# Performance work log

Measured on AMD Instinct MI355X. Metric: run time of the kernel, lower is better.

The kernel has to match this reference:

```python
import jax, jax.numpy as jnp
import numpy as np

MIN_LEN = 4      # g.min_word_length
MAX_LEN = 10     # g.max_word_length
THRESH = 0.05    # g.init_threshold
NEG = -1e9


def setup_inputs() -> dict:
    key = jax.random.key(0)
    ks = jax.random.split(key, 6)
    B, L, F, D, U, V = 16, 64, 60, 256, 600, 10000
    x = jax.random.normal(ks[0], (B, L, F), jnp.float32)            # batch dense feat matrix
    unit_feats = jax.random.normal(ks[1], (U, F), jnp.float32)      # per-unit features
    W = jax.random.normal(ks[2], (F, D), jnp.float32) * 0.1         # FeatEmbedding weight
    lengths = jax.random.randint(ks[3], (B,), MIN_LEN, L + 1)       # sentence lengths
    indexed_segments = jax.random.randint(ks[4], (V, MAX_LEN), 0, U)  # vocab -> unit ids
    vocab_length = jax.random.randint(ks[5], (V,), MIN_LEN, MAX_LEN + 1)
    return dict(x=x, unit_feats=unit_feats, W=W, lengths=lengths,
                indexed_segments=indexed_segments, vocab_length=vocab_length)


def reference(x, unit_feats, W, lengths, indexed_segments, vocab_length):
    B, L, _ = x.shape
    V, J = indexed_segments.shape
    # embedding: features -> char_emb space
    word_repr = x @ W                 # [B, L, D]
    unit_repr = unit_feats @ W        # [U, D]
    # cosine similarity between every segment position and every unit
    wn = word_repr / (jnp.linalg.norm(word_repr, axis=-1, keepdims=True) + 1e-8)
    un = unit_repr / (jnp.linalg.norm(unit_repr, axis=-1, keepdims=True) + 1e-8)
    sim = jnp.einsum('bld,ud->blu', wn, un)  # [B, L, U]
    # pad so span gathers past the end read zeros (masked later by `viable`)
    sim_pad = jnp.pad(sim, ((0, 0), (0, J), (0, 0)))
    # accumulate per-position unit scores along each vocab word's unit sequence
    acc = jnp.zeros((B, L, V), sim.dtype)
    per_len = []
    for j in range(J):  # fixed small loop over word-length positions
        # sim at start+j for unit indexed_segments[v, j] -> [B, L, V]
        s_j = sim_pad[:, j:j + L, :][:, :, indexed_segments[:, j]]
        acc = acc + s_j
        if j + 1 >= MIN_LEN:
            per_len.append(acc / (j + 1))  # length-normalized match score
    scores = jnp.stack(per_len, axis=2)  # [B, len_s=L, len_e=E, V]
    E = scores.shape[2]
    k = jnp.arange(E) + MIN_LEN                          # candidate word lengths
    ends = jnp.arange(L)[:, None] + k[None, :] - 1        # [L, E]
    viable = ends[None] < lengths[:, None, None]          # [B, L, E]
    len_match = vocab_length[None, None, None, :] == k[None, None, :, None]
    mask = viable[..., None] & len_match                  # [B, L, E, V]
    masked = jnp.where(mask, scores, NEG)
    # best vocab word per span candidate
    value = masked.max(axis=-1)                           # [B, L, E]
    matched_vocab = masked.argmax(axis=-1)                # [B, L, E]
    matched = value > THRESH
    # best span candidate per batch element (eval path: hard max)
    flat = value.reshape(B, -1)                           # [B, L*E]
    best_inds = flat.argmax(axis=-1)
    best_scores = flat.max(axis=-1)
    best_starts = best_inds // E
    best_ends = best_inds % E + best_starts + MIN_LEN - 1
    any_matched = matched.reshape(B, -1).any(axis=-1)
    best_vocab = jnp.take_along_axis(matched_vocab.reshape(B, -1), best_inds[:, None], axis=1)[:, 0]
    return best_scores, best_starts, best_ends, any_matched, best_vocab
```

## Files before the change

### kernel.cpp

```cpp
#include <hip/hip_runtime.h>
#include <math.h>

#define BB 16
#define LL 64
#define FF 60
#define DD 256
#define UU 600
#define VV 10000
#define JMAX 10
#define MINL 4
#define EE 7
#define NEG (-1e9f)
#define TH 0.05f
#define BCAP 10240

#define UNT_OFF   0
#define WNT_OFF   163840
#define SIM_OFF   425984
#define CNT_OFF   1040384
#define SRT_OFF   1040392
#define VAL_OFF   1613832
#define VOC_OFF   1628168

__global__ __launch_bounds__(256) void k_prep(const int* __restrict__ seg,
                                              const int* __restrict__ vlen,
                                              const float* __restrict__ x,
                                              const float* __restrict__ uf,
                                              const float* __restrict__ W,
                                              unsigned int* __restrict__ cnt,
                                              unsigned int* __restrict__ srt,
                                              float* __restrict__ unT,
                                              float* __restrict__ wnT) {
    __shared__ unsigned long long sP[4][2];
    __shared__ int wTab[4][8];
    __shared__ int sBase[8];
    int blk = blockIdx.x;
    if (blk < 40) {
        int tid  = threadIdx.x;
        int lane = tid & 63;
        int w    = tid >> 6;
        int v    = blk * 256 + tid;

        unsigned long long p0 = 0, p1 = 0;
        int lim = blk * 256;
        for (int i = tid; i < lim; i += 256) {
            int e2 = vlen[i] - MINL;
            if (e2 < 4) p0 += 1ull << (e2 * 16);
            else        p1 += 1ull << ((e2 - 4) * 16);
        }
#pragma unroll
        for (int m = 32; m > 0; m >>= 1) {
            p0 += __shfl_xor(p0, m, 64);
            p1 += __shfl_xor(p1, m, 64);
        }
        if (lane == 0) { sP[w][0] = p0; sP[w][1] = p1; }

        int e = (v < VV) ? (vlen[v] - MINL) : -1;
        unsigned long long below = (lane == 0) ? 0ull : (~0ull >> (64 - lane));
        unsigned long long mym = 0;
#pragma unroll
        for (int b2 = 0; b2 < EE; ++b2) {
            unsigned long long m = __ballot(e == b2);
            if (lane == 0) wTab[w][b2] = (int)__popcll(m);
            if (e == b2) mym = m;
        }
        __syncthreads();
        if (tid < EE) {
            unsigned long long q0 = sP[0][0] + sP[1][0] + sP[2][0] + sP[3][0];
            unsigned long long q1 = sP[0][1] + sP[1][1] + sP[2][1] + sP[3][1];
            int base = (tid < 4) ? (int)((q0 >> (tid * 16)) & 0xffffull)
                                 : (int)((q1 >> ((tid - 4) * 16)) & 0xffffull);
            sBase[tid] = base;
            if (blk == 39)
                cnt[tid] = (unsigned)(base + wTab[0][tid] + wTab[1][tid]
                                           + wTab[2][tid] + wTab[3][tid]);
        }
        __syncthreads();

        if (v < VV) {
            int prior = sBase[e];
#pragma unroll
            for (int w2 = 0; w2 < 4; ++w2) if (w2 < w) prior += wTab[w2][e];
            unsigned pos = (unsigned)(prior + (int)__popcll(mym & below));

            const int* s = seg + v * JMAX;
            unsigned int t[10];
#pragma unroll
            for (int j = 0; j < JMAX; ++j) t[j] = (unsigned int)(s[j] * 13 + j);
            unsigned int* dst = srt + ((size_t)e * BCAP + pos) * 8;
            uint4 qa, qb;
            qa.x = t[0] | (t[1] << 16);
            qa.y = t[2] | (t[3] << 16);
            qa.z = t[4] | (t[5] << 16);
            qa.w = t[6] | (t[7] << 16);
            qb.x = t[8] | (t[9] << 16);
            qb.y = (unsigned int)v;
            qb.z = 0; qb.w = 0;
            ((uint4*)dst)[0] = qa;
            ((uint4*)dst)[1] = qb;
        }
    } else {
        int w = threadIdx.x >> 6;
        int lane = threadIdx.x & 63;
        int id = (blk - 40) * 4 + w;
        const float* row;
        float* outB;
        int stride, col;
        if (id < UU) { row = uf + id * FF; outB = unT; stride = 640;  col = id; }
        else { int bl = id - UU; row = x + bl * FF; outB = wnT; stride = 1024; col = bl; }

        float r0 = 0.f, r1 = 0.f, r2 = 0.f, r3 = 0.f;
#pragma unroll 4
        for (int f = 0; f < FF; ++f) {
            float xv = row[f];
            r0 += xv * W[f * DD + lane];
            r1 += xv * W[f * DD + lane + 64];
            r2 += xv * W[f * DD + lane + 128];
            r3 += xv * W[f * DD + lane + 192];
        }
        float ss = r0 * r0 + r1 * r1 + r2 * r2 + r3 * r3;
#pragma unroll
        for (int m = 32; m > 0; m >>= 1) ss += __shfl_xor(ss, m, 64);
        float inv = 1.0f / (sqrtf(ss) + 1e-8f);
        outB[(lane      ) * stride + col] = r0 * inv;
        outB[(lane +  64) * stride + col] = r1 * inv;
        outB[(lane + 128) * stride + col] = r2 * inv;
        outB[(lane + 192) * stride + col] = r3 * inv;
    }
}

__global__ __launch_bounds__(320) void k_sim(const float* __restrict__ unT,
                                             const float* __restrict__ wnT,
                                             const int* __restrict__ lengths,
                                             float* __restrict__ sim) {
    int blk = blockIdx.x;
    int b  = blk >> 5;
    int r  = blk & 31;
    int l0 = (r >> 1) * 4;
    if (l0 >= lengths[b]) return;
    int uh = r & 1;
    int bl0 = b * 64 + l0;
    int u = uh * 320 + threadIdx.x;

    float a0 = 0.f, a1 = 0.f, a2 = 0.f, a3 = 0.f;
#pragma unroll 8
    for (int d = 0; d < DD; ++d) {
        float4 wv = *(const float4*)(wnT + d * 1024 + bl0);
        float v  = unT[d * 640 + u];
        a0 += wv.x * v;
        a1 += wv.y * v;
        a2 += wv.z * v;
        a3 += wv.w * v;
    }
    if (u < UU) {
        sim[(bl0 + 0) * UU + u] = a0;
        sim[(bl0 + 1) * UU + u] = a1;
        sim[(bl0 + 2) * UU + u] = a2;
        sim[(bl0 + 3) * UU + u] = a3;
    }
}

template<int K>
__device__ __forceinline__ void seg_pass4(const unsigned int* __restrict__ srt,
                                          const float* __restrict__ lds,
                                          int e, int r0, int r1, int lane, int wave,
                                          float (*redS)[8], int (*redV)[8]) {
    float s0 = -1e30f, s1 = -1e30f, s2 = -1e30f, s3 = -1e30f;
    int w0 = VV, w1 = VV, w2 = VV, w3 = VV;
    for (int p = r0 + lane; p < r1; p += 64) {
        const uint4* pp = (const uint4*)(srt + ((size_t)e * BCAP + p) * 8);
        uint4 qa = pp[0];
        uint4 qb = pp[1];
        unsigned int tw[5] = {qa.x, qa.y, qa.z, qa.w, qb.x};
        int v = (int)qb.y;
        float a0 = 0.f, a1 = 0.f, a2 = 0.f, a3 = 0.f;
#pragma unroll
        for (int j = 0; j < K; ++j) {
            int idx = (int)((tw[j >> 1] >> ((j & 1) * 16)) & 0xffffu);
            a0 += lds[idx];
            a1 += lds[idx + 1];
            a2 += lds[idx + 2];
            a3 += lds[idx + 3];
        }
        bool p0 = (a0 > s0) || (a0 == s0 && v < w0);
        bool p1 = (a1 > s1) || (a1 == s1 && v < w1);
        bool p2 = (a2 > s2) || (a2 == s2 && v < w2);
        bool p3 = (a3 > s3) || (a3 == s3 && v < w3);
        s0 = p0 ? a0 : s0;  w0 = p0 ? v : w0;
        s1 = p1 ? a1 : s1;  w1 = p1 ? v : w1;
        s2 = p2 ? a2 : s2;  w2 = p2 ? v : w2;
        s3 = p3 ? a3 : s3;  w3 = p3 ? v : w3;
    }
#pragma unroll
    for (int off = 32; off > 0; off >>= 1) {
        float os; int ov;
        os = __shfl_down(s0, off, 64); ov = __shfl_down(w0, off, 64);
        if (os > s0 || (os == s0 && ov < w0)) { s0 = os; w0 = ov; }
        os = __shfl_down(s1, off, 64); ov = __shfl_down(w1, off, 64);
        if (os > s1 || (os == s1 && ov < w1)) { s1 = os; w1 = ov; }
        os = __shfl_down(s2, off, 64); ov = __shfl_down(w2, off, 64);
        if (os > s2 || (os == s2 && ov < w2)) { s2 = os; w2 = ov; }
        os = __shfl_down(s3, off, 64); ov = __shfl_down(w3, off, 64);
        if (os > s3 || (os == s3 && ov < w3)) { s3 = os; w3 = ov; }
    }
    if (lane == 0) {
        redS[e * 4 + 0][wave] = s0; redV[e * 4 + 0][wave] = w0;
        redS[e * 4 + 1][wave] = s1; redV[e * 4 + 1][wave] = w1;
        redS[e * 4 + 2][wave] = s2; redV[e * 4 + 2][wave] = w2;
        redS[e * 4 + 3][wave] = s3; redV[e * 4 + 3][wave] = w3;
    }
}

__global__ __launch_bounds__(512, 4) void k_score(const float* __restrict__ sim,
                                                  const unsigned int* __restrict__ srt,
                                                  const unsigned int* __restrict__ cnt,
                                                  const int* __restrict__ lengths,
                                                  float* __restrict__ val,
                                                  int* __restrict__ voc) {
    __shared__ float lds[UU * 13];
    __shared__ float redS[28][8];
    __shared__ int   redV[28][8];

    int blk = blockIdx.x;
    int half = blk >> 8;
    int rest = blk & 255;
    int b  = rest >> 4;
    int l0 = (rest & 15) * 4;
    int tid = threadIdx.x;
    int len = lengths[b];

    if (l0 + MINL - 1 >= len) {
        if (tid < 28) {
            int e  = tid >> 2;
            int dl = tid & 3;
            int o = (half * BB * LL + b * 64 + l0 + dl) * EE + e;
            val[o] = NEG;
            voc[o] = 0;
        }
        return;
    }

    if (tid < 224) {
        redS[tid >> 3][tid & 7] = -1e30f;
        redV[tid >> 3][tid & 7] = VV;
    }
    for (int u = tid; u < UU; u += 512) {
#pragma unroll
        for (int r = 0; r < 13; ++r) {
            int m = l0 + r;
            lds[u * 13 + r] = (m < LL) ? sim[(b * 64 + m) * UU + u] : 0.0f;
        }
    }
    __syncthreads();

    int wave = tid >> 6, lane = tid & 63;

    unsigned nlo[EE], nhi[EE], Bw[EE];
    unsigned Wtot = 0;
#pragma unroll
    for (int e = 0; e < EE; ++e) {
        unsigned n = cnt[e];
        unsigned lo = half ? (n >> 1) : 0;
        unsigned hi = half ? n : (n >> 1);
        if (l0 + e + MINL - 1 >= len) { lo = 0; hi = 0; }
        nlo[e] = lo; nhi[e] = hi;
        Bw[e] = Wtot;
        Wtot += (hi - lo) * (unsigned)(e + MINL);
    }
    unsigned qlo = (unsigned)(((unsigned long long)Wtot * (unsigned)wave) >> 3);
    unsigned qhi = (unsigned)(((unsigned long long)Wtot * (unsigned)(wave + 1)) >> 3);

#pragma unroll
    for (int e = 0; e < EE; ++e) {
        unsigned K = (unsigned)(e + MINL);
        unsigned segw = (nhi[e] - nlo[e]) * K;
        unsigned Be = Bw[e];
        if (qhi <= Be || qlo >= Be + segw || segw == 0) continue;
        unsigned a = (qlo > Be) ? (qlo - Be) : 0;
        unsigned bb = qhi - Be; if (bb > segw) bb = segw;
        int r0 = (int)(nlo[e] + (a + K - 1) / K);
        int r1 = (int)(nlo[e] + (bb + K - 1) / K);
        if (r1 <= r0) continue;
        switch (e) {
            case 0: seg_pass4<4> (srt, lds, 0, r0, r1, lane, wave, redS, redV); break;
            case 1: seg_pass4<5> (srt, lds, 1, r0, r1, lane, wave, redS, redV); break;
            case 2: seg_pass4<6> (srt, lds, 2, r0, r1, lane, wave, redS, redV); break;
            case 3: seg_pass4<7> (srt, lds, 3, r0, r1, lane, wave, redS, redV); break;
            case 4: seg_pass4<8> (srt, lds, 4, r0, r1, lane, wave, redS, redV); break;
            case 5: seg_pass4<9> (srt, lds, 5, r0, r1, lane, wave, redS, redV); break;
            case 6: seg_pass4<10>(srt, lds, 6, r0, r1, lane, wave, redS, redV); break;
        }
    }
    __syncthreads();

    if (tid < 28) {
        int e  = tid >> 2;
        int dl = tid & 3;
        float s = redS[tid][0];
        int  vv = redV[tid][0];
#pragma unroll
        for (int w2 = 1; w2 < 8; ++w2) {
            float os = redS[tid][w2];
            int   ov = redV[tid][w2];
            if (os > s || (os == s && ov < vv)) { s = os; vv = ov; }
        }
        int lg = l0 + dl;
        int k = e + MINL;
        bool viable = (lg + k - 1) < len;
        float sn = s / (float)k;
        int o = (half * BB * LL + b * 64 + lg) * EE + e;
        val[o] = viable ? sn : NEG;
        voc[o] = viable ? vv : 0;
    }
}

__global__ __launch_bounds__(512) void k_final(const float* __restrict__ val,
                                               const int* __restrict__ voc,
                                               float* __restrict__ out) {
    __shared__ float sS[8];
    __shared__ int   sI[8];
    __shared__ int   sV[8];
    __shared__ int   sA[8];
    int b = blockIdx.x;
    int t = threadIdx.x;
    float s = -3e38f;
    int idx = 1 << 30;
    int vc = 0;
    int any = 0;
    if (t < LL * EE) {
        int o0 = b * LL * EE + t;
        int o1 = BB * LL * EE + o0;
        float s0 = val[o0], s1 = val[o1];
        int   v0 = voc[o0], v1 = voc[o1];
        bool sel = (s1 > s0) || (s1 == s0 && v1 < v0);
        s  = sel ? s1 : s0;
        vc = sel ? v1 : v0;
        idx = t;
        any = (s > TH) ? 1 : 0;
    }
#pragma unroll
    for (int off = 32; off > 0; off >>= 1) {
        float os = __shfl_down(s, off, 64);
        int   oi = __shfl_down(idx, off, 64);
        int   ov = __shfl_down(vc, off, 64);
        int   oa = __shfl_down(any, off, 64);
        if (os > s || (os == s && oi < idx)) { s = os; idx = oi; vc = ov; }
        any |= oa;
    }
    int w = t >> 6, lane = t & 63;
    if (lane == 0) { sS[w] = s; sI[w] = idx; sV[w] = vc; sA[w] = any; }
    __syncthreads();
    if (t == 0) {
        for (int w2 = 1; w2 < 8; ++w2) {
            float os = sS[w2];
            int   oi = sI[w2];
            if (os > s || (os == s && oi < idx)) { s = os; idx = oi; vc = sV[w2]; }
            any |= sA[w2];
        }
        int start = idx / EE;
        int e = idx - start * EE;
        int end = e + start + MINL - 1;
        out[b]      = s;
        out[16 + b] = (float)start;
        out[32 + b] = (float)end;
        out[48 + b] = any ? 1.0f : 0.0f;
        out[64 + b] = (float)vc;
    }
}

extern "C" void kernel_launch(void* const* d_in, const int* in_sizes, int n_in,
                              void* d_out, int out_size, void* d_ws, size_t ws_size,
                              hipStream_t stream) {
    const float* x       = (const float*)d_in[0];
    const float* uf      = (const float*)d_in[1];
    const float* W       = (const float*)d_in[2];
    const int*   lengths = (const int*)d_in[3];
    const int*   seg     = (const int*)d_in[4];
    const int*   vlen    = (const int*)d_in[5];
    float* out = (float*)d_out;
    float* ws  = (float*)d_ws;

    float*        unT = ws + UNT_OFF;
    float*        wnT = ws + WNT_OFF;
    float*        sim = ws + SIM_OFF;
    unsigned int* cnt = (unsigned int*)(ws + CNT_OFF);
    unsigned int* srt = (unsigned int*)(ws + SRT_OFF);
    float*        val = ws + VAL_OFF;
    int*          voc = (int*)(ws + VOC_OFF);

    k_prep<<<446, 256, 0, stream>>>(seg, vlen, x, uf, W, cnt, srt, unT, wnT);
    k_sim<<<512, 320, 0, stream>>>(unT, wnT, lengths, sim);
    k_score<<<512, 512, 0, stream>>>(sim, srt, cnt, lengths, val, voc);
    k_final<<<BB, 512, 0, stream>>>(val, voc, out);
}
```

Before: 128.6 us.

## Compact live (batch, start) tiles and split vocab across more blocks in k_score

A compacted table of live (batch, start-group) tiles is built in k_prep, from sentence lengths. k_score then maps its 512 blocks onto only those live tiles, splitting each tile's vocabulary range into up to 8 slices instead of a fixed 2. The aim is to stop dead blocks, which had nothing to do beyond positions past the sentence end, from idling while live blocks carry the full half-vocab load. k_final now reduces across a variable number of slices and writes NEG for non-viable spans. The trade-off is that each extra slice reloads the 13-row sim tile into LDS, the table is built serially by one thread, and the val/voc buffers grow.

```diff
diff --git a/kernel.cpp b/kernel.cpp
--- a/kernel.cpp
+++ b/kernel.cpp
@@ -13,21 +13,25 @@
 #define NEG (-1e9f)
 #define TH 0.05f
 #define BCAP 10240
+#define MAXS 8
 
 #define UNT_OFF   0
 #define WNT_OFF   163840
 #define SIM_OFF   425984
 #define CNT_OFF   1040384
-#define SRT_OFF   1040392
-#define VAL_OFF   1613832
-#define VOC_OFF   1628168
+#define QTB_OFF   1040392
+#define SRT_OFF   1040648
+#define VAL_OFF   1614088
+#define VOC_OFF   1671432
 
 __global__ __launch_bounds__(256) void k_prep(const int* __restrict__ seg,
                                               const int* __restrict__ vlen,
                                               const float* __restrict__ x,
                                               const float* __restrict__ uf,
                                               const float* __restrict__ W,
+                                              const int* __restrict__ lengths,
                                               unsigned int* __restrict__ cnt,
+                                              unsigned int* __restrict__ qtab,
                                               unsigned int* __restrict__ srt,
                                               float* __restrict__ unT,
                                               float* __restrict__ wnT) {
@@ -74,6 +78,15 @@
             if (blk == 39)
                 cnt[tid] = (unsigned)(base + wTab[0][tid] + wTab[1][tid]
                                            + wTab[2][tid] + wTab[3][tid]);
+        }
+        if (blk == 39 && tid == 64) {
+            int n = 0;
+            for (int b2 = 0; b2 < BB; ++b2) {
+                int len = lengths[b2];
+                for (int l0 = 0; l0 + MINL - 1 < len; l0 += 4)
+                    qtab[n++] = (unsigned)((b2 << 8) | l0);
+            }
+            cnt[7] = (unsigned)n;
         }
         __syncthreads();
 
@@ -214,31 +227,25 @@
 __global__ __launch_bounds__(512, 4) void k_score(const float* __restrict__ sim,
                                                   const unsigned int* __restrict__ srt,
                                                   const unsigned int* __restrict__ cnt,
-                                                  const int* __restrict__ lengths,
+                                                  const unsigned int* __restrict__ qtab,
                                                   float* __restrict__ val,
-                                                  int* __restrict__ voc) {
+                                                  int* __restrict__ voc,
+                                                  const int* __restrict__ lengths) {
     __shared__ float lds[UU * 13];
     __shared__ float redS[28][8];
     __shared__ int   redV[28][8];
 
-    int blk = blockIdx.x;
-    int half = blk >> 8;
-    int rest = blk & 255;
-    int b  = rest >> 4;
-    int l0 = (rest & 15) * 4;
     int tid = threadIdx.x;
+    unsigned nLive = cnt[7];
+    unsigned nS = 512u / nLive; if (nS > MAXS) nS = MAXS;
+    unsigned blk = blockIdx.x;
+    if (blk >= nLive * nS) return;
+    unsigned q  = blk % nLive;
+    unsigned sl = blk / nLive;
+    unsigned qt = qtab[q];
+    int b  = (int)(qt >> 8);
+    int l0 = (int)(qt & 255u);
     int len = lengths[b];
-
-    if (l0 + MINL - 1 >= len) {
-        if (tid < 28) {
-            int e  = tid >> 2;
-            int dl = tid & 3;
-            int o = (half * BB * LL + b * 64 + l0 + dl) * EE + e;
-            val[o] = NEG;
-            voc[o] = 0;
-        }
-        return;
-    }
 
     if (tid < 224) {
         redS[tid >> 3][tid & 7] = -1e30f;
@@ -260,8 +267,8 @@
 #pragma unroll
     for (int e = 0; e < EE; ++e) {
         unsigned n = cnt[e];
-        unsigned lo = half ? (n >> 1) : 0;
-        unsigned hi = half ? n : (n >> 1);
+        unsigned lo = (n * sl) / nS;
+        unsigned hi = (n * (sl + 1)) / nS;
         if (l0 + e + MINL - 1 >= len) { lo = 0; hi = 0; }
         nlo[e] = lo; nhi[e] = hi;
         Bw[e] = Wtot;
@@ -308,7 +315,7 @@
         int k = e + MINL;
         bool viable = (lg + k - 1) < len;
         float sn = s / (float)k;
-        int o = (half * BB * LL + b * 64 + lg) * EE + e;
+        int o = (((int)sl * BB + b) * LL + lg) * EE + e;
         val[o] = viable ? sn : NEG;
         voc[o] = viable ? vv : 0;
     }
@@ -316,6 +323,8 @@
 
 __global__ __launch_bounds__(512) void k_final(const float* __restrict__ val,
                                                const int* __restrict__ voc,
+                                               const int* __restrict__ lengths,
+                                               const unsigned int* __restrict__ cnt,
                                                float* __restrict__ out) {
     __shared__ float sS[8];
     __shared__ int   sI[8];
@@ -323,18 +332,30 @@
     __shared__ int   sA[8];
     int b = blockIdx.x;
     int t = threadIdx.x;
+    unsigned nLive = cnt[7];
+    unsigned nS = 512u / nLive; if (nS > MAXS) nS = MAXS;
+    int len = lengths[b];
     float s = -3e38f;
     int idx = 1 << 30;
     int vc = 0;
     int any = 0;
     if (t < LL * EE) {
-        int o0 = b * LL * EE + t;
-        int o1 = BB * LL * EE + o0;
-        float s0 = val[o0], s1 = val[o1];
-        int   v0 = voc[o0], v1 = voc[o1];
-        bool sel = (s1 > s0) || (s1 == s0 && v1 < v0);
-        s  = sel ? s1 : s0;
-        vc = sel ? v1 : v0;
+        int l = t / EE;
+        int e = t - l * EE;
+        bool viable = (l + e + MINL - 1) < len;
+        if (viable) {
+            int o0 = (b * LL + l) * EE + e;
+            s  = val[o0];
+            vc = voc[o0];
+            for (unsigned q2 = 1; q2 < nS; ++q2) {
+                int oq = (int)q2 * BB * LL * EE + o0;
+                float sq = val[oq];
+                int   vq = voc[oq];
+                if (sq > s || (sq == s && vq < vc)) { s = sq; vc = vq; }
+            }
+        } else {
+            s = NEG; vc = 0;
+        }
         idx = t;
         any = (s > TH) ? 1 : 0;
     }
@@ -380,16 +401,18 @@
     float* out = (float*)d_out;
     float* ws  = (float*)d_ws;
 
-    float*        unT = ws + UNT_OFF;
-    float*        wnT = ws + WNT_OFF;
-    float*        sim = ws + SIM_OFF;
-    unsigned int* cnt = (unsigned int*)(ws + CNT_OFF);
-    unsigned int* srt = (unsigned int*)(ws + SRT_OFF);
-    float*        val = ws + VAL_OFF;
-    int*          voc = (int*)(ws + VOC_OFF);
-
-    k_prep<<<446, 256, 0, stream>>>(seg, vlen, x, uf, W, cnt, srt, unT, wnT);
+    float*        unT  = ws + UNT_OFF;
+    float*        wnT  = ws + WNT_OFF;
+    float*        sim  = ws + SIM_OFF;
+    unsigned int* cnt  = (unsigned int*)(ws + CNT_OFF);
+    unsigned int* qtab = (unsigned int*)(ws + QTB_OFF);
+    unsigned int* srt  = (unsigned int*)(ws + SRT_OFF);
+    float*        val  = ws + VAL_OFF;
+    int*          voc  = (int*)(ws + VOC_OFF);
+
+    k_prep<<<446, 256, 0, stream>>>(seg, vlen, x, uf, W, lengths, cnt, qtab,
+                                    srt, unT, wnT);
     k_sim<<<512, 320, 0, stream>>>(unT, wnT, lengths, sim);
-    k_score<<<512, 512, 0, stream>>>(sim, srt, cnt, lengths, val, voc);
-    k_final<<<BB, 512, 0, stream>>>(val, voc, out);
-}
+    k_score<<<512, 512, 0, stream>>>(sim, srt, cnt, qtab, val, voc, lengths);
+    k_final<<<BB, 512, 0, stream>>>(val, voc, lengths, cnt, out);
+}
```

Measured after the change: 131.6 us. 2.3% more time.

## Fuse similarity computation into the scoring kernel and drop the sim buffer

Applied to the files above, without the earlier changes.

Removes the separate similarity kernel and its global sim buffer. Each scoring block now computes its 13-row by 600-unit slice of cosine similarities directly into shared memory from the normalized transposed embeddings. This saves one launch and the round trip of sim through global memory. In exchange, overlapping rows are recomputed by neighbouring blocks (about 13/4 times the work), and the dot-product loop is serial per thread with poor utilisation on the second unit pass.

```diff
diff --git a/kernel.cpp b/kernel.cpp
--- a/kernel.cpp
+++ b/kernel.cpp
@@ -16,11 +16,10 @@
 
 #define UNT_OFF   0
 #define WNT_OFF   163840
-#define SIM_OFF   425984
 #define CNT_OFF   1040384
 #define SRT_OFF   1040392
-#define VAL_OFF   1613832
-#define VOC_OFF   1628168
+#define VAL_OFF   1614088
+#define VOC_OFF   1628424
 
 __global__ __launch_bounds__(256) void k_prep(const int* __restrict__ seg,
                                               const int* __restrict__ vlen,
@@ -129,37 +128,6 @@
     }
 }
 
-__global__ __launch_bounds__(320) void k_sim(const float* __restrict__ unT,
-                                             const float* __restrict__ wnT,
-                                             const int* __restrict__ lengths,
-                                             float* __restrict__ sim) {
-    int blk = blockIdx.x;
-    int b  = blk >> 5;
-    int r  = blk & 31;
-    int l0 = (r >> 1) * 4;
-    if (l0 >= lengths[b]) return;
-    int uh = r & 1;
-    int bl0 = b * 64 + l0;
-    int u = uh * 320 + threadIdx.x;
-
-    float a0 = 0.f, a1 = 0.f, a2 = 0.f, a3 = 0.f;
-#pragma unroll 8
-    for (int d = 0; d < DD; ++d) {
-        float4 wv = *(const float4*)(wnT + d * 1024 + bl0);
-        float v  = unT[d * 640 + u];
-        a0 += wv.x * v;
-        a1 += wv.y * v;
-        a2 += wv.z * v;
-        a3 += wv.w * v;
-    }
-    if (u < UU) {
-        sim[(bl0 + 0) * UU + u] = a0;
-        sim[(bl0 + 1) * UU + u] = a1;
-        sim[(bl0 + 2) * UU + u] = a2;
-        sim[(bl0 + 3) * UU + u] = a3;
-    }
-}
-
 template<int K>
 __device__ __forceinline__ void seg_pass4(const unsigned int* __restrict__ srt,
                                           const float* __restrict__ lds,
@@ -211,12 +179,13 @@
     }
 }
 
-__global__ __launch_bounds__(512, 4) void k_score(const float* __restrict__ sim,
-                                                  const unsigned int* __restrict__ srt,
-                                                  const unsigned int* __restrict__ cnt,
-                                                  const int* __restrict__ lengths,
-                                                  float* __restrict__ val,
-                                                  int* __restrict__ voc) {
+__global__ __launch_bounds__(512, 4) void k_simscore(const float* __restrict__ unT,
+                                                     const float* __restrict__ wnT,
+                                                     const unsigned int* __restrict__ srt,
+                                                     const unsigned int* __restrict__ cnt,
+                                                     const int* __restrict__ lengths,
+                                                     float* __restrict__ val,
+                                                     int* __restrict__ voc) {
     __shared__ float lds[UU * 13];
     __shared__ float redS[28][8];
     __shared__ int   redV[28][8];
@@ -244,11 +213,21 @@
         redS[tid >> 3][tid & 7] = -1e30f;
         redV[tid >> 3][tid & 7] = VV;
     }
-    for (int u = tid; u < UU; u += 512) {
-#pragma unroll
-        for (int r = 0; r < 13; ++r) {
-            int m = l0 + r;
-            lds[u * 13 + r] = (m < LL) ? sim[(b * 64 + m) * UU + u] : 0.0f;
+    {
+        int bl0 = b * 64 + l0;
+        for (int u = tid; u < UU; u += 512) {
+            float acc[13];
+#pragma unroll
+            for (int r = 0; r < 13; ++r) acc[r] = 0.0f;
+            for (int d = 0; d < DD; ++d) {
+                float uv = unT[d * 640 + u];
+                const float* wrow = wnT + d * 1024 + bl0;
+#pragma unroll
+                for (int r = 0; r < 13; ++r) acc[r] += uv * wrow[r];
+            }
+#pragma unroll
+            for (int r = 0; r < 13; ++r)
+                lds[u * 13 + r] = (l0 + r < LL) ? acc[r] : 0.0f;
         }
     }
     __syncthreads();
@@ -382,14 +361,12 @@
 
     float*        unT = ws + UNT_OFF;
     float*        wnT = ws + WNT_OFF;
-    float*        sim = ws + SIM_OFF;
     unsigned int* cnt = (unsigned int*)(ws + CNT_OFF);
     unsigned int* srt = (unsigned int*)(ws + SRT_OFF);
     float*        val = ws + VAL_OFF;
     int*          voc = (int*)(ws + VOC_OFF);
 
     k_prep<<<446, 256, 0, stream>>>(seg, vlen, x, uf, W, cnt, srt, unT, wnT);
-    k_sim<<<512, 320, 0, stream>>>(unT, wnT, lengths, sim);
-    k_score<<<512, 512, 0, stream>>>(sim, srt, cnt, lengths, val, voc);
+    k_simscore<<<512, 512, 0, stream>>>(unT, wnT, srt, cnt, lengths, val, voc);
     k_final<<<BB, 512, 0, stream>>>(val, voc, out);
 }
```

Result: slower. 223.2 us (+73.6%).
